# Kernel optimization log

Measured on AMD Instinct MI355X. Metric: run time of the kernel, lower is better.

The kernel has to match this reference:

```python
import jax, jax.numpy as jnp
import numpy as np

B, TAPE, N, F = 128, 100000, 50000, 32

def setup_inputs() -> dict:
    key = jax.random.key(0)
    k1, k2, k3, k4 = jax.random.split(key, 4)
    tape = jax.random.normal(k1, (B, TAPE), dtype=jnp.float32)
    input_indices = jax.random.randint(k2, (N, F), 0, TAPE)
    # He init scaled by fan-in, padding slots (index==0) zeroed as in __init__
    weights = jax.random.normal(k3, (N, F), dtype=jnp.float32) * jnp.sqrt(2.0 / F)
    weights = jnp.where(input_indices == 0, 0.0, weights)
    bias = jnp.zeros((N,), dtype=jnp.float32)
    output_indices = jnp.arange(N)
    act_type = jax.random.randint(k4, (N,), 0, 2)
    return {"tape": tape, "weights": weights, "bias": bias,
            "input_indices": input_indices, "output_indices": output_indices,
            "act_type": act_type}

def reference(tape, weights, bias, input_indices, output_indices, act_type):
    # gather padded fan-in inputs: [B, N, F]
    gathered = tape[:, input_indices]
    # weighted sum over fan-in + bias: [B, N]
    x = jnp.einsum('bnf,nf->bn', gathered, weights) + bias
    # per-activation-type apply (two activation groups: relu / tanh)
    x = jnp.where(act_type == 0, jax.nn.relu(x), jnp.tanh(x))
    # scatter results back into tape
    return tape.at[:, output_indices].set(x)
```

## Files before the change

kernel.cpp:

```cpp
#include <hip/hip_runtime.h>
#include <hip/hip_bf16.h>
#include <cmath>

#define TAPE_SZ 100000
#define N_SZ    50000
#define F_SZ    32
#define B_SZ    128
#define NB      16

static __device__ __forceinline__ unsigned short f32_to_bf16(float f) {
    unsigned int u = __float_as_uint(f);
    u = (u + 0x7fffu + ((u >> 16) & 1u)) >> 16;
    return (unsigned short)u;
}

__global__ __launch_bounds__(256) void transpose_tape(const float* __restrict__ in,
                                                      unsigned short* __restrict__ outT,
                                                      float* __restrict__ out) {
    __shared__ float tile[32][129];
    const int x0 = blockIdx.x * 32;
    const int tx = threadIdx.x;
    const int ty = threadIdx.y;

    const bool tail = (x0 + tx >= N_SZ);
    #pragma unroll
    for (int yy = ty; yy < B_SZ; yy += 8) {
        const float v = in[(size_t)yy * TAPE_SZ + x0 + tx];
        tile[tx][yy] = v;
        if (tail) out[(size_t)yy * TAPE_SZ + x0 + tx] = v;
    }
    __syncthreads();

    const int tid = ty * 32 + tx;
    const int oct = tid & 15;
    const int xl0 = tid >> 4;
    #pragma unroll
    for (int xx = xl0; xx < 32; xx += 16) {
        const float* src = &tile[xx][oct * 8];
        union { unsigned short u[8]; uint4 q; } pk;
        #pragma unroll
        for (int k = 0; k < 8; ++k)
            pk.u[k] = f32_to_bf16(src[k]);
        *(uint4*)(outT + (size_t)(x0 + xx) * B_SZ + oct * 8) = pk.q;
    }
}

__global__ __launch_bounds__(256, 8) void gather_mm(const unsigned short* __restrict__ tapeT,
                                                    const float* __restrict__ weights,
                                                    const float* __restrict__ bias,
                                                    const int*   __restrict__ in_idx,
                                                    const int*   __restrict__ out_idx,
                                                    const int*   __restrict__ act_type,
                                                    float* __restrict__ out) {
    __shared__ int   s_idx[NB * 32];
    __shared__ float s_w[NB * 32];
    __shared__ float s_bias[NB];
    __shared__ int   s_act[NB];
    __shared__ int   s_oidx[NB];
    __shared__ float s_x[NB][132];

    const int tid = threadIdx.y * 16 + threadIdx.x;
    const int n0  = blockIdx.x * NB;

    #pragma unroll
    for (int t = tid; t < NB * 32; t += 256) {
        s_idx[t] = in_idx[(size_t)n0 * 32 + t];
        s_w[t]   = weights[(size_t)n0 * 32 + t];
    }
    if (tid < NB) {
        s_bias[tid] = bias[n0 + tid];
        s_act[tid]  = act_type[n0 + tid];
        s_oidx[tid] = out_idx[n0 + tid];
    }
    __syncthreads();

    const int nl = threadIdx.y;
    const int bx = threadIdx.x;
    float a0 = 0.f, a1 = 0.f, a2 = 0.f, a3 = 0.f, a4 = 0.f, a5 = 0.f, a6 = 0.f, a7 = 0.f;

    #pragma unroll 8
    for (int f = 0; f < 32; ++f) {
        const int   idx = s_idx[nl * 32 + f];
        const float w   = s_w[nl * 32 + f];
        const uint4 q   = *(const uint4*)(tapeT + (size_t)idx * B_SZ + bx * 8);
        a0 = fmaf(__uint_as_float(q.x << 16),          w, a0);
        a1 = fmaf(__uint_as_float(q.x & 0xffff0000u),  w, a1);
        a2 = fmaf(__uint_as_float(q.y << 16),          w, a2);
        a3 = fmaf(__uint_as_float(q.y & 0xffff0000u),  w, a3);
        a4 = fmaf(__uint_as_float(q.z << 16),          w, a4);
        a5 = fmaf(__uint_as_float(q.z & 0xffff0000u),  w, a5);
        a6 = fmaf(__uint_as_float(q.w << 16),          w, a6);
        a7 = fmaf(__uint_as_float(q.w & 0xffff0000u),  w, a7);
    }

    const float bz = s_bias[nl];
    a0 += bz; a1 += bz; a2 += bz; a3 += bz; a4 += bz; a5 += bz; a6 += bz; a7 += bz;
    if (s_act[nl] == 0) {
        a0 = fmaxf(a0, 0.f); a1 = fmaxf(a1, 0.f); a2 = fmaxf(a2, 0.f); a3 = fmaxf(a3, 0.f);
        a4 = fmaxf(a4, 0.f); a5 = fmaxf(a5, 0.f); a6 = fmaxf(a6, 0.f); a7 = fmaxf(a7, 0.f);
    } else {
        a0 = tanhf(a0); a1 = tanhf(a1); a2 = tanhf(a2); a3 = tanhf(a3);
        a4 = tanhf(a4); a5 = tanhf(a5); a6 = tanhf(a6); a7 = tanhf(a7);
    }
    *(float4*)(&s_x[nl][bx * 8])     = make_float4(a0, a1, a2, a3);
    *(float4*)(&s_x[nl][bx * 8 + 4]) = make_float4(a4, a5, a6, a7);
    __syncthreads();

    const int j    = tid & 15;
    const int brow = tid >> 4;
    const int oc   = s_oidx[j];
    #pragma unroll
    for (int k = 0; k < 8; ++k) {
        const int b = brow + k * 16;
        out[(size_t)b * TAPE_SZ + oc] = s_x[j][b];
    }
}

__global__ __launch_bounds__(128) void gather_fallback(const float* __restrict__ tape,
                                                       const float* __restrict__ weights,
                                                       const float* __restrict__ bias,
                                                       const int*   __restrict__ in_idx,
                                                       const int*   __restrict__ out_idx,
                                                       const int*   __restrict__ act_type,
                                                       float* __restrict__ out) {
    const int n = blockIdx.x;
    const int b = threadIdx.x;
    float acc = 0.f;
    for (int f = 0; f < F_SZ; ++f) {
        acc += tape[(size_t)b * TAPE_SZ + in_idx[(size_t)n * F_SZ + f]] *
               weights[(size_t)n * F_SZ + f];
    }
    acc += bias[n];
    acc = (act_type[n] == 0) ? fmaxf(acc, 0.f) : tanhf(acc);
    out[(size_t)b * TAPE_SZ + out_idx[n]] = acc;
}

__global__ __launch_bounds__(256) void copy_tail_fb(const float* __restrict__ tape,
                                                    float* __restrict__ out) {
    const int n4 = (TAPE_SZ - N_SZ) / 4;
    int i = blockIdx.x * blockDim.x + threadIdx.x;
    int b = blockIdx.y;
    if (i < n4) {
        const float4* src = (const float4*)(tape + (size_t)b * TAPE_SZ + N_SZ);
        float4*       dst = (float4*)(out  + (size_t)b * TAPE_SZ + N_SZ);
        dst[i] = src[i];
    }
}

extern "C" void kernel_launch(void* const* d_in, const int* in_sizes, int n_in,
                              void* d_out, int out_size, void* d_ws, size_t ws_size,
                              hipStream_t stream) {
    const float* tape    = (const float*)d_in[0];
    const float* weights = (const float*)d_in[1];
    const float* bias    = (const float*)d_in[2];
    const int*   in_idx  = (const int*)d_in[3];
    const int*   out_idx = (const int*)d_in[4];
    const int*   act     = (const int*)d_in[5];
    float*       out     = (float*)d_out;

    const size_t need = (size_t)TAPE_SZ * B_SZ * sizeof(unsigned short);
    if (ws_size >= need) {
        unsigned short* tapeT = (unsigned short*)d_ws;
        transpose_tape<<<dim3(TAPE_SZ / 32), dim3(32, 8), 0, stream>>>(tape, tapeT, out);
        gather_mm<<<dim3(N_SZ / NB), dim3(16, 16), 0, stream>>>(
            tapeT, weights, bias, in_idx, out_idx, act, out);
    } else {
        copy_tail_fb<<<dim3(((TAPE_SZ - N_SZ) / 4 + 255) / 256, B_SZ), 256, 0, stream>>>(tape, out);
        gather_fallback<<<dim3(N_SZ), 128, 0, stream>>>(
            tape, weights, bias, in_idx, out_idx, act, out);
    }
}
```

Measured before the change: 173.2 us.

## Split transposed bf16 tape into batch chunks and tile gather by node

The transposed bf16 tape is now stored as 8 batch chunks of 16 entries each, so each gather block reads only 32 bytes per index from one chunk. Block ids put the chunk in the low bits, so the 8 blocks sharing a node tile run next to each other and share cached index and weight loads. The intent is for each chunk's working set (about 3.2 MB) to stay resident in cache while many nodes gather from it. Each block now handles 128 nodes with transposed index and weight tiles in shared memory, and writes outputs straight to global memory without the shared staging step. The transpose kernel switches to float4 loads. The cost is that each index and weight row is reloaded once per chunk, and the scattered output writes are less coalesced.

```diff
diff --git a/kernel.cpp b/kernel.cpp
--- a/kernel.cpp
+++ b/kernel.cpp
@@ -1,12 +1,13 @@
 #include <hip/hip_runtime.h>
-#include <hip/hip_bf16.h>
 #include <cmath>
 
 #define TAPE_SZ 100000
 #define N_SZ    50000
 #define F_SZ    32
 #define B_SZ    128
-#define NB      16
+#define NCHUNK  8
+#define CB      16
+#define NT      128
 
 static __device__ __forceinline__ unsigned short f32_to_bf16(float f) {
     unsigned int u = __float_as_uint(f);
@@ -17,102 +18,124 @@
 __global__ __launch_bounds__(256) void transpose_tape(const float* __restrict__ in,
                                                       unsigned short* __restrict__ outT,
                                                       float* __restrict__ out) {
-    __shared__ float tile[32][129];
-    const int x0 = blockIdx.x * 32;
-    const int tx = threadIdx.x;
-    const int ty = threadIdx.y;
+    __shared__ float tile[32 * 133];
+    const int x0  = blockIdx.x * 32;
+    const int tid = threadIdx.x;
 
-    const bool tail = (x0 + tx >= N_SZ);
-    #pragma unroll
-    for (int yy = ty; yy < B_SZ; yy += 8) {
-        const float v = in[(size_t)yy * TAPE_SZ + x0 + tx];
-        tile[tx][yy] = v;
-        if (tail) out[(size_t)yy * TAPE_SZ + x0 + tx] = v;
+    {
+        const int xq = tid & 7;
+        const int b0 = tid >> 3;
+        const bool tail = (x0 + xq * 4 >= N_SZ);
+        #pragma unroll
+        for (int it = 0; it < 4; ++it) {
+            const int b = b0 + it * 32;
+            const float4 v = *(const float4*)(in + (size_t)b * TAPE_SZ + x0 + xq * 4);
+            tile[(xq * 4 + 0) * 133 + b] = v.x;
+            tile[(xq * 4 + 1) * 133 + b] = v.y;
+            tile[(xq * 4 + 2) * 133 + b] = v.z;
+            tile[(xq * 4 + 3) * 133 + b] = v.w;
+            if (tail) *(float4*)(out + (size_t)b * TAPE_SZ + x0 + xq * 4) = v;
+        }
     }
     __syncthreads();
 
-    const int tid = ty * 32 + tx;
-    const int oct = tid & 15;
-    const int xl0 = tid >> 4;
-    #pragma unroll
-    for (int xx = xl0; xx < 32; xx += 16) {
-        const float* src = &tile[xx][oct * 8];
-        union { unsigned short u[8]; uint4 q; } pk;
+    {
+        const int s  = tid & 63;
+        const int w  = tid >> 6;
+        const int h  = s & 1;
+        const int xr = s >> 1;
         #pragma unroll
-        for (int k = 0; k < 8; ++k)
-            pk.u[k] = f32_to_bf16(src[k]);
-        *(uint4*)(outT + (size_t)(x0 + xx) * B_SZ + oct * 8) = pk.q;
+        for (int j = 0; j < 2; ++j) {
+            const int c = w + 4 * j;
+            const float* src = &tile[xr * 133 + c * CB + h * 8];
+            union { unsigned short u[8]; uint4 q; } pk;
+            #pragma unroll
+            for (int k = 0; k < 8; ++k) pk.u[k] = f32_to_bf16(src[k]);
+            *(uint4*)(outT + ((size_t)c * TAPE_SZ + x0 + xr) * CB + h * 8) = pk.q;
+        }
     }
 }
 
-__global__ __launch_bounds__(256, 8) void gather_mm(const unsigned short* __restrict__ tapeT,
+__global__ __launch_bounds__(256, 4) void gather_mm(const unsigned short* __restrict__ tapeT,
                                                     const float* __restrict__ weights,
                                                     const float* __restrict__ bias,
                                                     const int*   __restrict__ in_idx,
                                                     const int*   __restrict__ out_idx,
                                                     const int*   __restrict__ act_type,
                                                     float* __restrict__ out) {
-    __shared__ int   s_idx[NB * 32];
-    __shared__ float s_w[NB * 32];
-    __shared__ float s_bias[NB];
-    __shared__ int   s_act[NB];
-    __shared__ int   s_oidx[NB];
-    __shared__ float s_x[NB][132];
+    __shared__ int   s_idxT[32 * 129];
+    __shared__ float s_wT[32 * 129];
+    __shared__ float s_bias[NT];
+    __shared__ int   s_act[NT];
+    __shared__ int   s_oidx[NT];
 
-    const int tid = threadIdx.y * 16 + threadIdx.x;
-    const int n0  = blockIdx.x * NB;
+    const int tid   = threadIdx.x;
+    const int c     = blockIdx.x & 7;
+    const int ntile = blockIdx.x >> 3;
+    const int n0    = ntile * NT;
+    const int nmax  = (N_SZ - n0 < NT) ? (N_SZ - n0) : NT;
 
-    #pragma unroll
-    for (int t = tid; t < NB * 32; t += 256) {
-        s_idx[t] = in_idx[(size_t)n0 * 32 + t];
-        s_w[t]   = weights[(size_t)n0 * 32 + t];
+    const uint4*  gi = (const uint4*)(in_idx)   + (size_t)n0 * 8;
+    const float4* gw = (const float4*)(weights) + (size_t)n0 * 8;
+    for (int i = tid; i < nmax * 8; i += 256) {
+        const int n  = i >> 3;
+        const int f0 = (i & 7) * 4;
+        const uint4  vi = gi[i];
+        const float4 vw = gw[i];
+        s_idxT[(f0 + 0) * 129 + n] = vi.x;
+        s_idxT[(f0 + 1) * 129 + n] = vi.y;
+        s_idxT[(f0 + 2) * 129 + n] = vi.z;
+        s_idxT[(f0 + 3) * 129 + n] = vi.w;
+        s_wT[(f0 + 0) * 129 + n] = vw.x;
+        s_wT[(f0 + 1) * 129 + n] = vw.y;
+        s_wT[(f0 + 2) * 129 + n] = vw.z;
+        s_wT[(f0 + 3) * 129 + n] = vw.w;
     }
-    if (tid < NB) {
+    if (tid < nmax) {
         s_bias[tid] = bias[n0 + tid];
         s_act[tid]  = act_type[n0 + tid];
         s_oidx[tid] = out_idx[n0 + tid];
     }
     __syncthreads();
 
-    const int nl = threadIdx.y;
-    const int bx = threadIdx.x;
-    float a0 = 0.f, a1 = 0.f, a2 = 0.f, a3 = 0.f, a4 = 0.f, a5 = 0.f, a6 = 0.f, a7 = 0.f;
-
-    #pragma unroll 8
-    for (int f = 0; f < 32; ++f) {
-        const int   idx = s_idx[nl * 32 + f];
-        const float w   = s_w[nl * 32 + f];
-        const uint4 q   = *(const uint4*)(tapeT + (size_t)idx * B_SZ + bx * 8);
-        a0 = fmaf(__uint_as_float(q.x << 16),          w, a0);
-        a1 = fmaf(__uint_as_float(q.x & 0xffff0000u),  w, a1);
-        a2 = fmaf(__uint_as_float(q.y << 16),          w, a2);
-        a3 = fmaf(__uint_as_float(q.y & 0xffff0000u),  w, a3);
-        a4 = fmaf(__uint_as_float(q.z << 16),          w, a4);
-        a5 = fmaf(__uint_as_float(q.z & 0xffff0000u),  w, a5);
-        a6 = fmaf(__uint_as_float(q.w << 16),          w, a6);
-        a7 = fmaf(__uint_as_float(q.w & 0xffff0000u),  w, a7);
-    }
-
-    const float bz = s_bias[nl];
-    a0 += bz; a1 += bz; a2 += bz; a3 += bz; a4 += bz; a5 += bz; a6 += bz; a7 += bz;
-    if (s_act[nl] == 0) {
-        a0 = fmaxf(a0, 0.f); a1 = fmaxf(a1, 0.f); a2 = fmaxf(a2, 0.f); a3 = fmaxf(a3, 0.f);
-        a4 = fmaxf(a4, 0.f); a5 = fmaxf(a5, 0.f); a6 = fmaxf(a6, 0.f); a7 = fmaxf(a7, 0.f);
-    } else {
-        a0 = tanhf(a0); a1 = tanhf(a1); a2 = tanhf(a2); a3 = tanhf(a3);
-        a4 = tanhf(a4); a5 = tanhf(a5); a6 = tanhf(a6); a7 = tanhf(a7);
-    }
-    *(float4*)(&s_x[nl][bx * 8])     = make_float4(a0, a1, a2, a3);
-    *(float4*)(&s_x[nl][bx * 8 + 4]) = make_float4(a4, a5, a6, a7);
-    __syncthreads();
-
-    const int j    = tid & 15;
-    const int brow = tid >> 4;
-    const int oc   = s_oidx[j];
-    #pragma unroll
-    for (int k = 0; k < 8; ++k) {
-        const int b = brow + k * 16;
-        out[(size_t)b * TAPE_SZ + oc] = s_x[j][b];
+    const int oct = tid & 1;
+    const int nl  = tid >> 1;
+    if (nl < nmax) {
+        const unsigned short* base = tapeT + (size_t)c * TAPE_SZ * CB + oct * 8;
+        float a0 = 0.f, a1 = 0.f, a2 = 0.f, a3 = 0.f, a4 = 0.f, a5 = 0.f, a6 = 0.f, a7 = 0.f;
+        #pragma unroll 8
+        for (int f = 0; f < 32; ++f) {
+            const int   idx = s_idxT[f * 129 + nl];
+            const float w   = s_wT[f * 129 + nl];
+            const uint4 q   = *(const uint4*)(base + (size_t)idx * CB);
+            a0 = fmaf(__uint_as_float(q.x << 16),         w, a0);
+            a1 = fmaf(__uint_as_float(q.x & 0xffff0000u), w, a1);
+            a2 = fmaf(__uint_as_float(q.y << 16),         w, a2);
+            a3 = fmaf(__uint_as_float(q.y & 0xffff0000u), w, a3);
+            a4 = fmaf(__uint_as_float(q.z << 16),         w, a4);
+            a5 = fmaf(__uint_as_float(q.z & 0xffff0000u), w, a5);
+            a6 = fmaf(__uint_as_float(q.w << 16),         w, a6);
+            a7 = fmaf(__uint_as_float(q.w & 0xffff0000u), w, a7);
+        }
+        const float bz = s_bias[nl];
+        a0 += bz; a1 += bz; a2 += bz; a3 += bz; a4 += bz; a5 += bz; a6 += bz; a7 += bz;
+        if (s_act[nl] == 0) {
+            a0 = fmaxf(a0, 0.f); a1 = fmaxf(a1, 0.f); a2 = fmaxf(a2, 0.f); a3 = fmaxf(a3, 0.f);
+            a4 = fmaxf(a4, 0.f); a5 = fmaxf(a5, 0.f); a6 = fmaxf(a6, 0.f); a7 = fmaxf(a7, 0.f);
+        } else {
+            a0 = tanhf(a0); a1 = tanhf(a1); a2 = tanhf(a2); a3 = tanhf(a3);
+            a4 = tanhf(a4); a5 = tanhf(a5); a6 = tanhf(a6); a7 = tanhf(a7);
+        }
+        const int oc = s_oidx[nl];
+        const int bb = c * CB + oct * 8;
+        out[(size_t)(bb + 0) * TAPE_SZ + oc] = a0;
+        out[(size_t)(bb + 1) * TAPE_SZ + oc] = a1;
+        out[(size_t)(bb + 2) * TAPE_SZ + oc] = a2;
+        out[(size_t)(bb + 3) * TAPE_SZ + oc] = a3;
+        out[(size_t)(bb + 4) * TAPE_SZ + oc] = a4;
+        out[(size_t)(bb + 5) * TAPE_SZ + oc] = a5;
+        out[(size_t)(bb + 6) * TAPE_SZ + oc] = a6;
+        out[(size_t)(bb + 7) * TAPE_SZ + oc] = a7;
     }
 }
 
@@ -158,11 +181,12 @@
     const int*   act     = (const int*)d_in[5];
     float*       out     = (float*)d_out;
 
-    const size_t need = (size_t)TAPE_SZ * B_SZ * sizeof(unsigned short);
+    const size_t need = (size_t)NCHUNK * TAPE_SZ * CB * sizeof(unsigned short);
     if (ws_size >= need) {
         unsigned short* tapeT = (unsigned short*)d_ws;
-        transpose_tape<<<dim3(TAPE_SZ / 32), dim3(32, 8), 0, stream>>>(tape, tapeT, out);
-        gather_mm<<<dim3(N_SZ / NB), dim3(16, 16), 0, stream>>>(
+        transpose_tape<<<dim3(TAPE_SZ / 32), dim3(256), 0, stream>>>(tape, tapeT, out);
+        const int ntiles = (N_SZ + NT - 1) / NT;
+        gather_mm<<<dim3(ntiles * NCHUNK), dim3(256), 0, stream>>>(
             tapeT, weights, bias, in_idx, out_idx, act, out);
     } else {
         copy_tail_fb<<<dim3(((TAPE_SZ - N_SZ) / 4 + 255) / 256, B_SZ), 256, 0, stream>>>(tape, out);
```

New measurement: 187.5 us. 1.08x slower.
